# Kernel optimization log

Measured on AMD Instinct MI355X. Metric: run time of the kernel, lower is better.

Reference implementation:

```python
import jax, jax.numpy as jnp
import numpy as np

N_NODES = 50000
N_EDGES = 800000


def setup_inputs() -> dict:
    key = jax.random.key(0)
    ks = jax.random.split(key, 10)
    x = jax.random.normal(ks[0], (N_NODES, 256), dtype=jnp.float32)
    edge_index = jax.random.randint(ks[1], (2, N_EDGES), 0, N_NODES, dtype=jnp.int64)
    edge_attr = jax.random.uniform(ks[2], (N_EDGES,), dtype=jnp.float32)
    def glorot(k, fan_in, fan_out):
        s = jnp.sqrt(6.0 / (fan_in + fan_out))
        return jax.random.uniform(k, (fan_in, fan_out), minval=-s, maxval=s, dtype=jnp.float32)
    W1 = glorot(ks[3], 256, 512); b1 = jnp.zeros((512,), jnp.float32)
    W2 = glorot(ks[4], 512, 256); b2 = jnp.zeros((256,), jnp.float32)
    W3 = glorot(ks[5], 256, 128); b3 = jnp.zeros((128,), jnp.float32)
    return {"x": x, "edge_index": edge_index, "edge_attr": edge_attr,
            "W1": W1, "b1": b1, "W2": W2, "b2": b2, "W3": W3, "b3": b3}


def _gcn_norm(edge_index, edge_attr, num_nodes):
    # PyG GCNConv default: add self-loops (weight 1), symmetric normalization.
    loops = jnp.arange(num_nodes, dtype=edge_index.dtype)
    src = jnp.concatenate([edge_index[0], loops])
    dst = jnp.concatenate([edge_index[1], loops])
    w = jnp.concatenate([edge_attr, jnp.ones((num_nodes,), edge_attr.dtype)])
    deg = jax.ops.segment_sum(w, dst, num_segments=num_nodes)
    dinv = jnp.where(deg > 0, jax.lax.rsqrt(deg), 0.0)
    norm = dinv[src] * w * dinv[dst]  # [E+N]
    return src, dst, norm


def _gcn_conv(h, W, b, src, dst, norm, num_nodes):
    h = h @ W                                   # [N, Dout] linear transform
    msg = h[src] * norm[:, None]                # gather + per-edge scale
    out = jax.ops.segment_sum(msg, dst, num_segments=num_nodes)  # scatter-add
    return out + b


def reference(x, edge_index, edge_attr, W1, b1, W2, b2, W3, b3):
    src, dst, norm = _gcn_norm(edge_index, edge_attr, N_NODES)
    h = jax.nn.relu(_gcn_conv(x, W1, b1, src, dst, norm, N_NODES))
    # dropout is identity in eval mode (reference runs with training=False)
    h = jax.nn.relu(_gcn_conv(h, W2, b2, src, dst, norm, N_NODES))
    h = _gcn_conv(h, W3, b3, src, dst, norm, N_NODES)
    return h.reshape(-1, h.shape[1])
```

## Files before the change

### kernel.cpp

```cpp
#include <hip/hip_runtime.h>
#include <cstdint>
#include <cstddef>

typedef unsigned short u16;
typedef unsigned int u32;

#define NN 50000
#define NE 800000

typedef __attribute__((ext_vector_type(8))) short bf16x8;
typedef __attribute__((ext_vector_type(4))) float f32x4;

__device__ __forceinline__ u16 f2bf(float f) {
  union { float f; u32 i; } v; v.f = f;
  return (u16)((v.i + 0x7FFFu + ((v.i >> 16) & 1u)) >> 16);
}
__device__ __forceinline__ void bf2x2(u32 w, float& a, float& b) {
  union { u32 i; float f; } lo, hi;
  lo.i = w << 16; hi.i = w & 0xFFFF0000u;
  a = lo.f; b = hi.f;
}
__device__ __forceinline__ void unpack8(const uint4& q, float* f) {
  bf2x2(q.x, f[0], f[1]); bf2x2(q.y, f[2], f[3]);
  bf2x2(q.z, f[4], f[5]); bf2x2(q.w, f[6], f[7]);
}

#define XGROUPS (NN * 256 / 4)
#define NA_B 782
#define T_B 14455

__global__ void k_hist_cast(const int* __restrict__ dst,
                            int* __restrict__ cnt, int* __restrict__ slot,
                            const float* __restrict__ x, const float* __restrict__ W1,
                            const float* __restrict__ W2, const float* __restrict__ W3,
                            u16* __restrict__ xb, u16* __restrict__ Wt1,
                            u16* __restrict__ Wt2, u16* __restrict__ Wt3) {
  int b = blockIdx.x;
  int q = b / 18, r = b - q * 18;
  if (r == 17) {
    if (q >= NA_B) return;
    int ebase = q * 1024 + threadIdx.x;
    int ds[4]; bool ok[4];
#pragma unroll
    for (int u = 0; u < 4; u++) {
      int e = ebase + u * 256;
      ok[u] = e < NE;
      ds[u] = ok[u] ? dst[e] : 0;
    }
    int sl[4];
#pragma unroll
    for (int u = 0; u < 4; u++)
      if (ok[u]) sl[u] = atomicAdd(&cnt[ds[u]], 1);
#pragma unroll
    for (int u = 0; u < 4; u++)
      if (ok[u]) slot[ebase + u * 256] = sl[u];
  } else {
    int ci = b - q;
    int i = ci * 256 + threadIdx.x;
    if (i < XGROUPS) {
      float4 f = ((const float4*)x)[i];
      uint2 u;
      u.x = (u32)f2bf(f.x) | ((u32)f2bf(f.y) << 16);
      u.y = (u32)f2bf(f.z) | ((u32)f2bf(f.w) << 16);
      ((uint2*)xb)[i] = u;
    } else {
      int j = i - XGROUPS;
      if (j < 131072) {
        int k = j >> 9, n = j & 511;
        Wt1[n * 256 + k] = f2bf(W1[j]);
      } else if (j < 262144) {
        int j2 = j - 131072;
        int k = j2 >> 8, n = j2 & 255;
        Wt2[n * 512 + k] = f2bf(W2[j2]);
      } else if (j < 294912) {
        int j2 = j - 262144;
        int k = j2 >> 7, n = j2 & 127;
        Wt3[n * 256 + k] = f2bf(W3[j2]);
      }
    }
  }
}

__global__ void k_scan_part(const int* __restrict__ cnt, int* __restrict__ bsum, int n) {
  __shared__ int s[256];
  int i = blockIdx.x * 256 + threadIdx.x;
  s[threadIdx.x] = (i < n) ? cnt[i] : 0;
  __syncthreads();
  for (int o = 128; o > 0; o >>= 1) {
    if (threadIdx.x < o) s[threadIdx.x] += s[threadIdx.x + o];
    __syncthreads();
  }
  if (threadIdx.x == 0) bsum[blockIdx.x] = s[0];
}
__global__ void k_scan_fin(const int* __restrict__ cnt, const int* __restrict__ bsum,
                           int* __restrict__ rowptr, int n) {
  __shared__ int s[256];
  __shared__ int pre[256];
  int t = threadIdx.x;
  int i = blockIdx.x * 256 + t;
  pre[t] = (t < blockIdx.x) ? bsum[t] : 0;
  s[t] = (i < n) ? cnt[i] : 0;
  __syncthreads();
  for (int o = 128; o > 0; o >>= 1) {
    if (t < o) pre[t] += pre[t + o];
    __syncthreads();
  }
  if (t == 0) {
    int run = pre[0];
    for (int j = 0; j < 256; j++) { int v = s[j]; s[j] = run; run += v; }
  }
  __syncthreads();
  if (i < n) rowptr[i] = s[t];
}
__global__ void k_fill(const int* __restrict__ src, const int* __restrict__ dst,
                       const float* __restrict__ w, const int* __restrict__ rowptr,
                       const int* __restrict__ slot, uint2* __restrict__ edges, int E) {
  int e = blockIdx.x * 256 + threadIdx.x;
  if (e < E) {
    int d = dst[e];
    uint2 ev;
    ev.x = (u32)src[e];
    ev.y = __float_as_uint(w[e]);
    edges[rowptr[d] + slot[e]] = ev;
  }
}

__global__ __launch_bounds__(256) void k_sortrow(
    uint2* __restrict__ edges, const int* __restrict__ rowptr,
    const int* __restrict__ cnt, float* __restrict__ dinv, int n) {
  int wave = threadIdx.x >> 6, lane = threadIdx.x & 63;
  int row = blockIdx.x * 4 + wave;
  if (row >= n) return;
  int p = rowptr[row], c = cnt[row];
  if (c <= 64) {
    u32 kc = 0xFFFFFFFFu, kw = 0xFFFFFFFFu;
    if (lane < c) { uint2 e = edges[p + lane]; kc = e.x; kw = e.y; }
#pragma unroll
    for (int k = 2; k <= 64; k <<= 1) {
#pragma unroll
      for (int j = k >> 1; j > 0; j >>= 1) {
        u32 oc = __shfl_xor(kc, j, 64);
        u32 ow = __shfl_xor(kw, j, 64);
        bool up = ((lane & k) == 0);
        bool lower = ((lane & j) == 0);
        bool gt = (kc > oc) || (kc == oc && kw > ow);
        bool lt = (kc < oc) || (kc == oc && kw < ow);
        bool swap = up ? (lower ? gt : lt) : (lower ? lt : gt);
        if (swap) { kc = oc; kw = ow; }
      }
    }
    float s = (lane < c) ? __uint_as_float(kw) : 0.f;
#pragma unroll
    for (int off = 1; off < 64; off <<= 1) s += __shfl_xor(s, off, 64);
    if (lane < c) { uint2 e; e.x = kc; e.y = kw; edges[p + lane] = e; }
    if (lane == 0) dinv[row] = rsqrtf(1.0f + s);
  } else {
    if (lane == 0) {
      for (int i = 1; i < c; i++) {
        uint2 key = edges[p + i];
        int j2 = i - 1;
        while (j2 >= 0) {
          uint2 a = edges[p + j2];
          bool gt = (a.x > key.x) || (a.x == key.x && a.y > key.y);
          if (!gt) break;
          edges[p + j2 + 1] = a; j2--;
        }
        edges[p + j2 + 1] = key;
      }
      float s = 0.f;
      for (int i = 0; i < c; i++) s += __uint_as_float(edges[p + i].y);
      dinv[row] = rsqrtf(1.0f + s);
    }
  }
}

__global__ __launch_bounds__(256) void k_val(
    uint2* __restrict__ edges, const int* __restrict__ rowptr,
    const int* __restrict__ cnt, const float* __restrict__ dinv, int n) {
  int wave = threadIdx.x >> 6, lane = threadIdx.x & 63;
  int row = blockIdx.x * 4 + wave;
  if (row >= n) return;
  int p = rowptr[row], c = cnt[row];
  float dr = dinv[row];
  for (int l = lane; l < c; l += 64) {
    uint2 e = edges[p + l];
    float w = __uint_as_float(e.y);
    e.y = __float_as_uint(dinv[(int)e.x] * w * dr);
    edges[p + l] = e;
  }
}

template <int D, int OUTF32, int RELU, int HASB, int U>
__global__ __launch_bounds__(128) void k_agg(
    const u16* __restrict__ H, const int* __restrict__ rowptr,
    const int* __restrict__ cnt, const uint2* __restrict__ edges,
    const float* __restrict__ dinv,
    const float* __restrict__ bias, void* __restrict__ outv) {
  constexpr int RL = D / 8;
  constexpr int EPW = 64 / RL;
  int wave = threadIdx.x >> 6, lane = threadIdx.x & 63;
  int node = blockIdx.x * 2 + wave;
  if (node >= NN) return;
  const int sub = lane / RL;
  const int rl = lane & (RL - 1);
  const int base = rl * 8;
  float acc[8] = {};
  if (sub == 0) {
    float dv = dinv[node];
    float sw = dv * dv;
    uint4 q = *(const uint4*)(H + (size_t)node * D + base);
    float f[8]; unpack8(q, f);
#pragma unroll
    for (int j = 0; j < 8; j++) acc[j] = sw * f[j];
  }
  const int p = rowptr[node], c = cnt[node];
  for (int e0 = 0; e0 < c; e0 += EPW * U) {
    uint4 q[U];
    float v[U];
#pragma unroll
    for (int u = 0; u < U; u++) {
      int id = e0 + sub + u * EPW;
      bool ok = id < c;
      uint2 ev = edges[p + (ok ? id : 0)];
      v[u] = ok ? __uint_as_float(ev.y) : 0.f;
      int cs = ok ? (int)ev.x : node;
      q[u] = *(const uint4*)(H + (size_t)cs * D + base);
    }
#pragma unroll
    for (int u = 0; u < U; u++) {
      float f[8]; unpack8(q[u], f);
#pragma unroll
      for (int j = 0; j < 8; j++) acc[j] += v[u] * f[j];
    }
  }
#pragma unroll
  for (int j = 0; j < 8; j++) {
#pragma unroll
    for (int off = RL; off < 64; off <<= 1)
      acc[j] += __shfl_xor(acc[j], off, 64);
  }
  if (sub == 0) {
#pragma unroll
    for (int j = 0; j < 8; j++) {
      float v2 = acc[j];
      if (HASB) v2 += bias[base + j];
      if (RELU) v2 = fmaxf(v2, 0.f);
      acc[j] = v2;
    }
    if (OUTF32) {
      float* o = (float*)outv + (size_t)node * D + base;
      float4 f0 = {acc[0], acc[1], acc[2], acc[3]};
      float4 f1 = {acc[4], acc[5], acc[6], acc[7]};
      *(float4*)o = f0;
      *(float4*)(o + 4) = f1;
    } else {
      u16* o = (u16*)outv + (size_t)node * D + base;
      uint4 u;
      u.x = (u32)f2bf(acc[0]) | ((u32)f2bf(acc[1]) << 16);
      u.y = (u32)f2bf(acc[2]) | ((u32)f2bf(acc[3]) << 16);
      u.z = (u32)f2bf(acc[4]) | ((u32)f2bf(acc[5]) << 16);
      u.w = (u32)f2bf(acc[6]) | ((u32)f2bf(acc[7]) << 16);
      *(uint4*)o = u;
    }
  }
}

template <int RELU, int HASB, int NYB>
__global__ __launch_bounds__(512) void k_gemm(
    const u16* __restrict__ A, const u16* __restrict__ Bt,
    const float* __restrict__ bias, u16* __restrict__ C, int M, int Nd, int K) {
  __shared__ u16 As[256 * 64];
  __shared__ u16 Bs[128 * 64];
  const int tid = threadIdx.x;
  const int wave = tid >> 6, lane = tid & 63;
  const int nwg = gridDim.x;
  const int orig = blockIdx.x;
  const int xcd = orig & 7;
  const int q = nwg >> 3, r = nwg & 7;
  const int wgid = (xcd < r ? xcd * (q + 1) : r * (q + 1) + (xcd - r) * q) + (orig >> 3);
  const int m0 = (wgid / NYB) * 256, n0 = (wgid % NYB) * 128;
  const int wr = wave >> 1, wc = wave & 1;
  f32x4 acc[4][4] = {};

  for (int k0 = 0; k0 < K; k0 += 64) {
#pragma unroll
    for (int i = 0; i < 4; i++) {
      int rr = i * 64 + wave * 8 + (lane >> 3);
      int rg = m0 + rr; rg = rg < M ? rg : M - 1;
      const u16* ga = A + (size_t)rg * K + k0 + (lane & 7) * 8;
      __builtin_amdgcn_global_load_lds(
          (const __attribute__((address_space(1))) void*)ga,
          (__attribute__((address_space(3))) void*)&As[(i * 64 + wave * 8) * 64], 16, 0, 0);
    }
#pragma unroll
    for (int i = 0; i < 2; i++) {
      int rr = i * 64 + wave * 8 + (lane >> 3);
      int ng = n0 + rr;
      const u16* gb = Bt + (size_t)ng * K + k0 + (lane & 7) * 8;
      __builtin_amdgcn_global_load_lds(
          (const __attribute__((address_space(1))) void*)gb,
          (__attribute__((address_space(3))) void*)&Bs[(i * 64 + wave * 8) * 64], 16, 0, 0);
    }
    __syncthreads();
#pragma unroll
    for (int kk = 0; kk < 2; kk++) {
      bf16x8 af[4], bfr[4];
#pragma unroll
      for (int mi = 0; mi < 4; mi++)
        af[mi] = *(const bf16x8*)&As[(wr * 64 + mi * 16 + (lane & 15)) * 64 + kk * 32 + (lane >> 4) * 8];
#pragma unroll
      for (int ni = 0; ni < 4; ni++)
        bfr[ni] = *(const bf16x8*)&Bs[(wc * 64 + ni * 16 + (lane & 15)) * 64 + kk * 32 + (lane >> 4) * 8];
#pragma unroll
      for (int mi = 0; mi < 4; mi++)
#pragma unroll
        for (int ni = 0; ni < 4; ni++)
          acc[mi][ni] = __builtin_amdgcn_mfma_f32_16x16x32_bf16(af[mi], bfr[ni], acc[mi][ni], 0, 0, 0);
    }
    __syncthreads();
  }
  const int nb = n0 + wc * 64 + (lane & 15);
  float bv[4];
#pragma unroll
  for (int ni = 0; ni < 4; ni++) bv[ni] = HASB ? bias[nb + ni * 16] : 0.f;
#pragma unroll
  for (int mi = 0; mi < 4; mi++) {
#pragma unroll
    for (int rr = 0; rr < 4; rr++) {
      int row = m0 + wr * 64 + mi * 16 + (lane >> 4) * 4 + rr;
      if (row < M) {
#pragma unroll
        for (int ni = 0; ni < 4; ni++) {
          float v = acc[mi][ni][rr] + bv[ni];
          if (RELU) v = fmaxf(v, 0.f);
          C[(size_t)row * Nd + nb + ni * 16] = f2bf(v);
        }
      }
    }
  }
}

extern "C" void kernel_launch(void* const* d_in, const int* in_sizes, int n_in,
                              void* d_out, int out_size, void* d_ws, size_t ws_size,
                              hipStream_t stream) {
  const float* x  = (const float*)d_in[0];
  const int*   ei = (const int*)d_in[1];
  const float* ea = (const float*)d_in[2];
  const float* W1 = (const float*)d_in[3];
  const float* b1 = (const float*)d_in[4];
  const float* W2 = (const float*)d_in[5];
  const float* b2 = (const float*)d_in[6];
  const float* W3 = (const float*)d_in[7];
  const float* b3 = (const float*)d_in[8];
  const int* e_src = ei;
  const int* e_dst = ei + NE;

  size_t off = 0;
  auto carve = [&](size_t bytes) -> void* {
    void* r = (char*)d_ws + off;
    off += (bytes + 255) & ~(size_t)255;
    return r;
  };
  int*   counts = (int*)carve(NN * 4);
  float* dinv   = (float*)carve(NN * 4);
  int*   rowptr = (int*)carve(NN * 4);
  int*   bsum   = (int*)carve(256 * 4);
  int*   slot   = (int*)carve((size_t)NE * 4);
  uint2* edges  = (uint2*)carve((size_t)NE * 8);
  u16*   Wt1    = (u16*)carve(512 * 256 * 2);
  u16*   Wt2    = (u16*)carve(256 * 512 * 2);
  u16*   Wt3    = (u16*)carve(128 * 256 * 2);
  u16*   R0     = (u16*)carve((size_t)NN * 256 * 2);
  u16*   R1     = (u16*)carve((size_t)NN * 256 * 2);
  u16*   R2     = (u16*)carve((size_t)NN * 512 * 2);

  const int NB_N = (NN + 255) / 256;
  const int NB_E = (NE + 255) / 256;
  const int ROW_B = (NN + 3) / 4;
  const int AGG_B = (NN + 1) / 2;

  hipMemsetAsync(counts, 0, (size_t)NN * 4, stream);

  k_hist_cast<<<T_B, 256, 0, stream>>>(
      e_dst, counts, slot, x, W1, W2, W3, R0, Wt1, Wt2, Wt3);
  k_scan_part<<<NB_N, 256, 0, stream>>>(counts, bsum, NN);
  k_scan_fin<<<NB_N, 256, 0, stream>>>(counts, bsum, rowptr, NN);
  k_fill<<<NB_E, 256, 0, stream>>>(e_src, e_dst, ea, rowptr, slot, edges, NE);
  k_sortrow<<<ROW_B, 256, 0, stream>>>(edges, rowptr, counts, dinv, NN);
  k_val<<<ROW_B, 256, 0, stream>>>(edges, rowptr, counts, dinv, NN);

  k_agg<256, 0, 0, 0, 4><<<AGG_B, 128, 0, stream>>>(R0, rowptr, counts, edges, dinv, nullptr, R1);
  k_gemm<1, 1, 4><<<196 * 4, 512, 0, stream>>>(R1, Wt1, b1, R2, NN, 512, 256);
  k_gemm<0, 0, 2><<<196 * 2, 512, 0, stream>>>(R2, Wt2, nullptr, R0, NN, 256, 512);
  k_agg<256, 0, 1, 1, 4><<<AGG_B, 128, 0, stream>>>(R0, rowptr, counts, edges, dinv, b2, R1);
  k_gemm<0, 0, 1><<<196 * 1, 512, 0, stream>>>(R1, Wt3, nullptr, R0, NN, 128, 256);
  k_agg<128, 1, 0, 1, 4><<<AGG_B, 128, 0, stream>>>(R0, rowptr, counts, edges, dinv, b3, d_out);
}
```

Measured before the change: 342.0 us.

## Pack degree count and fixed-point weight sum into one 64-bit atomic

The histogram kernel now does a single 64-bit atomicAdd that accumulates both the edge count (high bits) and a fixed-point edge-weight sum (low 40 bits). This lets the scan kernel compute dinv directly and the fill kernel write fully normalized edge values, so the k_val pass and the per-row reduction in the sort kernel are removed. The cost is 64-bit atomics instead of 32-bit ones, a larger memset, and a fixed-point approximation of the weight sum. The sort now orders on normalized weights, but ties on the source index only occur for duplicate edges.

```diff
diff --git a/kernel.cpp b/kernel.cpp
--- a/kernel.cpp
+++ b/kernel.cpp
@@ -4,6 +4,7 @@
 
 typedef unsigned short u16;
 typedef unsigned int u32;
+typedef unsigned long long u64;
 
 #define NN 50000
 #define NE 800000
@@ -28,9 +29,11 @@
 #define XGROUPS (NN * 256 / 4)
 #define NA_B 782
 #define T_B 14455
-
-__global__ void k_hist_cast(const int* __restrict__ dst,
-                            int* __restrict__ cnt, int* __restrict__ slot,
+#define WSCALE 33554432.0f
+#define WMASK  0xFFFFFFFFFFull
+
+__global__ void k_hist_cast(const int* __restrict__ dst, const float* __restrict__ w,
+                            u64* __restrict__ degpack, int* __restrict__ slot,
                             const float* __restrict__ x, const float* __restrict__ W1,
                             const float* __restrict__ W2, const float* __restrict__ W3,
                             u16* __restrict__ xb, u16* __restrict__ Wt1,
@@ -40,17 +43,19 @@
   if (r == 17) {
     if (q >= NA_B) return;
     int ebase = q * 1024 + threadIdx.x;
-    int ds[4]; bool ok[4];
+    int ds[4]; u64 inc[4]; bool ok[4];
 #pragma unroll
     for (int u = 0; u < 4; u++) {
       int e = ebase + u * 256;
       ok[u] = e < NE;
       ds[u] = ok[u] ? dst[e] : 0;
+      u32 wfix = ok[u] ? (u32)(w[e] * WSCALE + 0.5f) : 0u;
+      inc[u] = (1ULL << 40) | (u64)wfix;
     }
     int sl[4];
 #pragma unroll
     for (int u = 0; u < 4; u++)
-      if (ok[u]) sl[u] = atomicAdd(&cnt[ds[u]], 1);
+      if (ok[u]) sl[u] = (int)(atomicAdd(&degpack[ds[u]], inc[u]) >> 40);
 #pragma unroll
     for (int u = 0; u < 4; u++)
       if (ok[u]) slot[ebase + u * 256] = sl[u];
@@ -81,10 +86,10 @@
   }
 }
 
-__global__ void k_scan_part(const int* __restrict__ cnt, int* __restrict__ bsum, int n) {
+__global__ void k_scan_part(const u64* __restrict__ degpack, int* __restrict__ bsum, int n) {
   __shared__ int s[256];
   int i = blockIdx.x * 256 + threadIdx.x;
-  s[threadIdx.x] = (i < n) ? cnt[i] : 0;
+  s[threadIdx.x] = (i < n) ? (int)(degpack[i] >> 40) : 0;
   __syncthreads();
   for (int o = 128; o > 0; o >>= 1) {
     if (threadIdx.x < o) s[threadIdx.x] += s[threadIdx.x + o];
@@ -92,14 +97,17 @@
   }
   if (threadIdx.x == 0) bsum[blockIdx.x] = s[0];
 }
-__global__ void k_scan_fin(const int* __restrict__ cnt, const int* __restrict__ bsum,
-                           int* __restrict__ rowptr, int n) {
+__global__ void k_scan_fin(const u64* __restrict__ degpack, const int* __restrict__ bsum,
+                           int* __restrict__ rowptr, int* __restrict__ counts,
+                           float* __restrict__ dinv, int n) {
   __shared__ int s[256];
   __shared__ int pre[256];
   int t = threadIdx.x;
   int i = blockIdx.x * 256 + t;
+  u64 dp = (i < n) ? degpack[i] : 0ull;
+  int c = (int)(dp >> 40);
   pre[t] = (t < blockIdx.x) ? bsum[t] : 0;
-  s[t] = (i < n) ? cnt[i] : 0;
+  s[t] = c;
   __syncthreads();
   for (int o = 128; o > 0; o >>= 1) {
     if (t < o) pre[t] += pre[t + o];
@@ -110,24 +118,30 @@
     for (int j = 0; j < 256; j++) { int v = s[j]; s[j] = run; run += v; }
   }
   __syncthreads();
-  if (i < n) rowptr[i] = s[t];
+  if (i < n) {
+    rowptr[i] = s[t];
+    counts[i] = c;
+    float wsum = (float)(dp & WMASK) * (1.0f / WSCALE);
+    dinv[i] = rsqrtf(1.0f + wsum);
+  }
 }
 __global__ void k_fill(const int* __restrict__ src, const int* __restrict__ dst,
                        const float* __restrict__ w, const int* __restrict__ rowptr,
-                       const int* __restrict__ slot, uint2* __restrict__ edges, int E) {
+                       const int* __restrict__ slot, const float* __restrict__ dinv,
+                       uint2* __restrict__ edges, int E) {
   int e = blockIdx.x * 256 + threadIdx.x;
   if (e < E) {
-    int d = dst[e];
+    int d = dst[e], s0 = src[e];
     uint2 ev;
-    ev.x = (u32)src[e];
-    ev.y = __float_as_uint(w[e]);
+    ev.x = (u32)s0;
+    ev.y = __float_as_uint(dinv[s0] * w[e] * dinv[d]);
     edges[rowptr[d] + slot[e]] = ev;
   }
 }
 
 __global__ __launch_bounds__(256) void k_sortrow(
     uint2* __restrict__ edges, const int* __restrict__ rowptr,
-    const int* __restrict__ cnt, float* __restrict__ dinv, int n) {
+    const int* __restrict__ cnt, int n) {
   int wave = threadIdx.x >> 6, lane = threadIdx.x & 63;
   int row = blockIdx.x * 4 + wave;
   if (row >= n) return;
@@ -149,11 +163,7 @@
         if (swap) { kc = oc; kw = ow; }
       }
     }
-    float s = (lane < c) ? __uint_as_float(kw) : 0.f;
-#pragma unroll
-    for (int off = 1; off < 64; off <<= 1) s += __shfl_xor(s, off, 64);
     if (lane < c) { uint2 e; e.x = kc; e.y = kw; edges[p + lane] = e; }
-    if (lane == 0) dinv[row] = rsqrtf(1.0f + s);
   } else {
     if (lane == 0) {
       for (int i = 1; i < c; i++) {
@@ -167,26 +177,7 @@
         }
         edges[p + j2 + 1] = key;
       }
-      float s = 0.f;
-      for (int i = 0; i < c; i++) s += __uint_as_float(edges[p + i].y);
-      dinv[row] = rsqrtf(1.0f + s);
-    }
-  }
-}
-
-__global__ __launch_bounds__(256) void k_val(
-    uint2* __restrict__ edges, const int* __restrict__ rowptr,
-    const int* __restrict__ cnt, const float* __restrict__ dinv, int n) {
-  int wave = threadIdx.x >> 6, lane = threadIdx.x & 63;
-  int row = blockIdx.x * 4 + wave;
-  if (row >= n) return;
-  int p = rowptr[row], c = cnt[row];
-  float dr = dinv[row];
-  for (int l = lane; l < c; l += 64) {
-    uint2 e = edges[p + l];
-    float w = __uint_as_float(e.y);
-    e.y = __float_as_uint(dinv[(int)e.x] * w * dr);
-    edges[p + l] = e;
+    }
   }
 }
 
@@ -361,33 +352,33 @@
     off += (bytes + 255) & ~(size_t)255;
     return r;
   };
-  int*   counts = (int*)carve(NN * 4);
-  float* dinv   = (float*)carve(NN * 4);
-  int*   rowptr = (int*)carve(NN * 4);
-  int*   bsum   = (int*)carve(256 * 4);
-  int*   slot   = (int*)carve((size_t)NE * 4);
-  uint2* edges  = (uint2*)carve((size_t)NE * 8);
-  u16*   Wt1    = (u16*)carve(512 * 256 * 2);
-  u16*   Wt2    = (u16*)carve(256 * 512 * 2);
-  u16*   Wt3    = (u16*)carve(128 * 256 * 2);
-  u16*   R0     = (u16*)carve((size_t)NN * 256 * 2);
-  u16*   R1     = (u16*)carve((size_t)NN * 256 * 2);
-  u16*   R2     = (u16*)carve((size_t)NN * 512 * 2);
+  u64*   degpack = (u64*)carve(NN * 8);
+  int*   counts  = (int*)carve(NN * 4);
+  float* dinv    = (float*)carve(NN * 4);
+  int*   rowptr  = (int*)carve(NN * 4);
+  int*   bsum    = (int*)carve(256 * 4);
+  int*   slot    = (int*)carve((size_t)NE * 4);
+  uint2* edges   = (uint2*)carve((size_t)NE * 8);
+  u16*   Wt1     = (u16*)carve(512 * 256 * 2);
+  u16*   Wt2     = (u16*)carve(256 * 512 * 2);
+  u16*   Wt3     = (u16*)carve(128 * 256 * 2);
+  u16*   R0      = (u16*)carve((size_t)NN * 256 * 2);
+  u16*   R1      = (u16*)carve((size_t)NN * 256 * 2);
+  u16*   R2      = (u16*)carve((size_t)NN * 512 * 2);
 
   const int NB_N = (NN + 255) / 256;
   const int NB_E = (NE + 255) / 256;
   const int ROW_B = (NN + 3) / 4;
   const int AGG_B = (NN + 1) / 2;
 
-  hipMemsetAsync(counts, 0, (size_t)NN * 4, stream);
+  hipMemsetAsync(degpack, 0, (size_t)NN * 8, stream);
 
   k_hist_cast<<<T_B, 256, 0, stream>>>(
-      e_dst, counts, slot, x, W1, W2, W3, R0, Wt1, Wt2, Wt3);
-  k_scan_part<<<NB_N, 256, 0, stream>>>(counts, bsum, NN);
-  k_scan_fin<<<NB_N, 256, 0, stream>>>(counts, bsum, rowptr, NN);
-  k_fill<<<NB_E, 256, 0, stream>>>(e_src, e_dst, ea, rowptr, slot, edges, NE);
-  k_sortrow<<<ROW_B, 256, 0, stream>>>(edges, rowptr, counts, dinv, NN);
-  k_val<<<ROW_B, 256, 0, stream>>>(edges, rowptr, counts, dinv, NN);
+      e_dst, ea, degpack, slot, x, W1, W2, W3, R0, Wt1, Wt2, Wt3);
+  k_scan_part<<<NB_N, 256, 0, stream>>>(degpack, bsum, NN);
+  k_scan_fin<<<NB_N, 256, 0, stream>>>(degpack, bsum, rowptr, counts, dinv, NN);
+  k_fill<<<NB_E, 256, 0, stream>>>(e_src, e_dst, ea, rowptr, slot, dinv, edges, NE);
+  k_sortrow<<<ROW_B, 256, 0, stream>>>(edges, rowptr, counts, NN);
 
   k_agg<256, 0, 0, 0, 4><<<AGG_B, 128, 0, stream>>>(R0, rowptr, counts, edges, dinv, nullptr, R1);
   k_gemm<1, 1, 4><<<196 * 4, 512, 0, stream>>>(R1, Wt1, b1, R2, NN, 512, 256);
```

New measurement: 337.3 us. About the same (-1.4%).
